# Kernel tuning notes

Measured on AMD Instinct MI355X. Metric: run time of the kernel, lower is better.

The kernel has to match this reference:

```python
import jax, jax.numpy as jnp
from jax import lax
import numpy as np

BATCH, SEQ_LEN, ENC_IN, C_OUT = 16, 512, 32, 32
N_ORDER = 256           # window_size
MULTISCALE = (1, 2, 4)
MODES = min(32, SEQ_LEN // 2)  # = 32


def make_hippo(N, dt):
    """HiPPO-LegT transition, bilinear (Tustin) discretization, Legendre eval matrix."""
    Q = np.arange(N, dtype=np.float64)
    R = (2 * Q + 1)[:, None]
    j, i = np.meshgrid(Q, Q)
    A = np.where(i < j, -1.0, (-1.0) ** (i - j + 1)) * R
    B = (-1.0) ** Q[:, None] * R                      # [N,1]
    I = np.eye(N)
    M = I - (dt / 2.0) * A
    Ad = np.linalg.solve(M, I + (dt / 2.0) * A)
    Bd = np.linalg.solve(M, dt * B).squeeze(-1)       # [N]
    vals = np.arange(0.0, 1.0, dt)
    x = 1.0 - 2.0 * vals
    P = np.zeros((N, len(vals)))
    P[0] = 1.0
    if N > 1:
        P[1] = x
    for n in range(1, N - 1):
        P[n + 1] = ((2 * n + 1) * x * P[n] - n * P[n - 1]) / (n + 1)
    E = P.T                                           # [len(vals), N]
    return Ad.astype(np.float32), Bd.astype(np.float32), E.astype(np.float32)


def setup_inputs():
    key = jax.random.key(0)
    ks = jax.random.split(key, 12)
    inp = {}
    inp['x_enc'] = jax.random.normal(ks[0], (BATCH, SEQ_LEN, ENC_IN), jnp.float32)
    inp['x_mark_enc'] = jax.random.normal(ks[1], (BATCH, SEQ_LEN, 4), jnp.float32)
    inp['x_dec'] = jax.random.normal(ks[2], (BATCH, SEQ_LEN, ENC_IN), jnp.float32)
    inp['x_mark_dec'] = jax.random.normal(ks[3], (BATCH, SEQ_LEN, 4), jnp.float32)
    inp['affine_weight'] = jnp.ones((1, 1, ENC_IN), jnp.float32)
    inp['affine_bias'] = jnp.zeros((1, 1, ENC_IN), jnp.float32)
    scale = 1.0 / (N_ORDER * N_ORDER)
    for s in range(3):
        inp[f'wr{s}'] = scale * jax.random.uniform(ks[4 + 2 * s], (N_ORDER, N_ORDER, MODES), jnp.float32)
        inp[f'wi{s}'] = scale * jax.random.uniform(ks[5 + 2 * s], (N_ORDER, N_ORDER, MODES), jnp.float32)
    inp['mlp_w'] = 0.1 * jax.random.normal(ks[10], (1, 3), jnp.float32)
    inp['mlp_b'] = jnp.zeros((1,), jnp.float32)
    inp['proj_w'] = 0.02 * jax.random.normal(ks[11], (ENC_IN, C_OUT), jnp.float32)
    inp['proj_b'] = jnp.zeros((C_OUT,), jnp.float32)
    for s, m in enumerate(MULTISCALE):
        A, Bv, E = make_hippo(N_ORDER, 1.0 / SEQ_LEN / m)
        inp[f'A{s}'] = jnp.asarray(A)
        inp[f'Bv{s}'] = jnp.asarray(Bv)
        inp[f'E{s}'] = jnp.asarray(E)
    return inp


def _hippo_scan(x, A, Bv):
    # x: [B, L, C] -> cs: [L, B, C, N]; c_t = A c_{t-1} + B f_t (applied on last dim)
    B_, L, C = x.shape
    c0 = jnp.zeros((B_, C, A.shape[0]), x.dtype)
    At = A.T
    def step(c, f):                      # f: [B, C]
        c = c @ At + f[..., None] * Bv
        return c, c
    _, cs = lax.scan(step, c0, jnp.transpose(x, (1, 0, 2)))
    return cs


def _spectral_conv(xc, wr, wi):
    # xc: [B, C, N, L]; keep first MODES rfft bins, complex channel mix over N, irfft
    L = xc.shape[-1]
    xf = jnp.fft.rfft(xc)                                # [B,C,N,L//2+1] complex64
    W = (wr + 1j * wi).astype(jnp.complex64)             # [N,N,MODES]
    out = jnp.einsum('bjix,iox->bjox', xf[..., :MODES], W)
    out_ft = jnp.pad(out, ((0, 0), (0, 0), (0, 0), (0, L // 2 + 1 - MODES)))
    return jnp.fft.irfft(out_ft, n=L)                    # [B,C,N,L]


def _forward(x_enc, affine_weight, affine_bias, specs, mlp_w, mlp_b, proj_w, proj_b, hippos):
    means = lax.stop_gradient(jnp.mean(x_enc, axis=1, keepdims=True))
    xc = x_enc - means
    stdev = lax.stop_gradient(jnp.sqrt(jnp.var(xc, axis=1, keepdims=True) + 1e-5))
    x = xc / stdev
    x = x * affine_weight + affine_bias                  # [B, L, C]
    pred_len = SEQ_LEN
    decs = []
    for (wr, wi), (A, Bv, E) in zip(specs, hippos):
        # multiscale slice x[:, -m*pred_len:] clips to full seq_len since pred_len==seq_len
        cs = _hippo_scan(x, A, Bv)                       # [L,B,C,N]
        x_in_c = jnp.transpose(cs, (1, 2, 3, 0))         # [B,C,N,L]
        out1 = _spectral_conv(x_in_c, wr, wi)            # [B,C,N,L]
        x_dec_c = out1[..., pred_len - 1]                # [B,C,N]
        dec = x_dec_c @ E[-pred_len:, :].T               # [B,C,pred_len]
        decs.append(dec)
    stacked = jnp.stack(decs, axis=-1)                   # [B,C,P,3]
    y = stacked @ mlp_w[0] + mlp_b[0]                    # Linear(3,1) + squeeze -> [B,C,P]
    y = jnp.transpose(y, (0, 2, 1))                      # [B,P,C]
    y = (y - affine_bias) / (affine_weight + 1e-10)
    y = y * stdev + means
    return y @ proj_w + proj_b                           # OutputBlock: per-step channel projection


def reference(x_enc, x_mark_enc, x_dec, x_mark_dec, affine_weight, affine_bias,
              wr0, wi0, wr1, wi1, wr2, wi2, mlp_w, mlp_b, proj_w, proj_b,
              A0, Bv0, E0, A1, Bv1, E1, A2, Bv2, E2):
    specs = [(wr0, wi0), (wr1, wi1), (wr2, wi2)]
    hippos = [(A0, Bv0, E0), (A1, Bv1, E1), (A2, Bv2, E2)]
    return _forward(x_enc, affine_weight, affine_bias, specs, mlp_w, mlp_b, proj_w, proj_b, hippos)
```

## Files before the change

### kernel.cpp

```cpp
#include <hip/hip_runtime.h>
#include <math.h>

#define SEQ 512
#define NORD 256
#define MODES 32
#define KBIG (NORD*MODES*2)
#define PI_F 3.14159265358979323846f

typedef _Float16 half8 __attribute__((ext_vector_type(8)));
typedef float floatx4 __attribute__((ext_vector_type(4)));


struct GJob {
  const float* A; const float* B; float* C; const float* scale_ptr;
  int M, N, lda, k0, k1, atomic;
};
struct GJobs { GJob j[6]; };

__global__ __launch_bounds__(256) void gemm32_k(GJobs P) {
  GJob jb = P.j[blockIdx.z];
  int col0 = blockIdx.x * 32;
  int row0 = blockIdx.y * 32;
  if (row0 >= jb.M || col0 >= jb.N) return;
  __shared__ float As[64][34];
  __shared__ float Bs[64][36];
  int tid = threadIdx.x;
  int tx = tid & 15, ty = tid >> 4;
  const float* A = jb.A; const float* B = jb.B;
  int M = jb.M, N = jb.N, lda = jb.lda;
  int kcA = (tid & 15) * 4, rA = tid >> 4;
  int ccB = (tid & 7) * 4, kkB = tid >> 3;
  int gr0 = row0 + rA, gr1 = row0 + rA + 16;
  const float4 z4 = make_float4(0.f, 0.f, 0.f, 0.f);
  float4 a0, a1, b0, b1;
  {
    int kb = jb.k0;
    a0 = (gr0 < M) ? *(const float4*)&A[(size_t)gr0 * lda + kb + kcA] : z4;
    a1 = (gr1 < M) ? *(const float4*)&A[(size_t)gr1 * lda + kb + kcA] : z4;
    b0 = *(const float4*)&B[(size_t)(kb + kkB) * N + col0 + ccB];
    b1 = *(const float4*)&B[(size_t)(kb + kkB + 32) * N + col0 + ccB];
  }
  float acc00 = 0.f, acc01 = 0.f, acc10 = 0.f, acc11 = 0.f;
  for (int kb = jb.k0; kb < jb.k1; kb += 64) {
    As[kcA+0][rA] = a0.x; As[kcA+1][rA] = a0.y; As[kcA+2][rA] = a0.z; As[kcA+3][rA] = a0.w;
    As[kcA+0][rA+16] = a1.x; As[kcA+1][rA+16] = a1.y; As[kcA+2][rA+16] = a1.z; As[kcA+3][rA+16] = a1.w;
    *(float4*)&Bs[kkB][ccB] = b0;
    *(float4*)&Bs[kkB+32][ccB] = b1;
    __syncthreads();
    if (kb + 64 < jb.k1) {
      int kn = kb + 64;
      a0 = (gr0 < M) ? *(const float4*)&A[(size_t)gr0 * lda + kn + kcA] : z4;
      a1 = (gr1 < M) ? *(const float4*)&A[(size_t)gr1 * lda + kn + kcA] : z4;
      b0 = *(const float4*)&B[(size_t)(kn + kkB) * N + col0 + ccB];
      b1 = *(const float4*)&B[(size_t)(kn + kkB + 32) * N + col0 + ccB];
    }
    #pragma unroll
    for (int k = 0; k < 64; k++) {
      float2 av = *(float2*)&As[k][ty * 2];
      float2 bv = *(float2*)&Bs[k][tx * 2];
      acc00 += av.x * bv.x; acc01 += av.x * bv.y;
      acc10 += av.y * bv.x; acc11 += av.y * bv.y;
    }
    __syncthreads();
  }
  float sc = jb.scale_ptr ? *jb.scale_ptr : 1.f;
  int gr = row0 + ty * 2, gc = col0 + tx * 2;
  float v00 = acc00 * sc, v01 = acc01 * sc, v10 = acc10 * sc, v11 = acc11 * sc;
  if (jb.atomic) {
    if (gr < M)     { atomicAdd(&jb.C[(size_t)gr * N + gc], v00);     atomicAdd(&jb.C[(size_t)gr * N + gc + 1], v01); }
    if (gr + 1 < M) { atomicAdd(&jb.C[(size_t)(gr+1) * N + gc], v10); atomicAdd(&jb.C[(size_t)(gr+1) * N + gc + 1], v11); }
  } else {
    if (gr < M)     { jb.C[(size_t)gr * N + gc] = v00;     jb.C[(size_t)gr * N + gc + 1] = v01; }
    if (gr + 1 < M) { jb.C[(size_t)(gr+1) * N + gc] = v10; jb.C[(size_t)(gr+1) * N + gc + 1] = v11; }
  }
}


__global__ __launch_bounds__(256) void prep2_k(const float* __restrict__ x_enc,
                                               const float* __restrict__ aw,
                                               const float* __restrict__ ab,
                                               float* __restrict__ F,
                                               float* __restrict__ stats,
                                               const float* A0, const float* A1, const float* A2,
                                               const float* B0, const float* B1, const float* B2,
                                               const float* E0, const float* E1, const float* E2,
                                               float* R, float* Kry, float* Et, float* Z,
                                               const float* wr0, const float* wi0,
                                               const float* wr1, const float* wi1,
                                               const float* wr2, const float* wi2,
                                               _Float16* __restrict__ Wt) {
  __shared__ float tile[32][33];
  __shared__ float ws1[4], ws2[4];
  __shared__ float mean_s, istd_s;
  int bid = blockIdx.x;
  int tid = threadIdx.x;
  if (bid < 512) {
    int row = bid;
    int b = row >> 5, c = row & 31;
    const float* xp = x_enc + (size_t)b * SEQ * 32 + c;
    float v0 = xp[(size_t)tid * 32];
    float v1 = xp[(size_t)(tid + 256) * 32];
    float s = v0 + v1, s2 = v0 * v0 + v1 * v1;
    for (int off = 32; off; off >>= 1) {
      s  += __shfl_down(s,  off, 64);
      s2 += __shfl_down(s2, off, 64);
    }
    int wid = tid >> 6, lane = tid & 63;
    if (lane == 0) { ws1[wid] = s; ws2[wid] = s2; }
    __syncthreads();
    if (tid == 0) {
      float t1 = ws1[0] + ws1[1] + ws1[2] + ws1[3];
      float t2 = ws2[0] + ws2[1] + ws2[2] + ws2[3];
      float mean = t1 / 512.f;
      float var = t2 / 512.f - mean * mean;
      float sd = sqrtf(var + 1e-5f);
      mean_s = mean; istd_s = 1.f / sd;
      stats[row] = mean; stats[512 + row] = sd;
    }
    __syncthreads();
    float w = aw[c], bb = ab[c];
    float m = mean_s, is = istd_s;
    F[(size_t)row * SEQ + tid]       = (v0 - m) * is * w + bb;
    F[(size_t)row * SEQ + tid + 256] = (v1 - m) * is * w + bb;
  } else if (bid < 704) {
    int b2 = bid - 512;
    int scl = b2 >> 6, t = b2 & 63;
    int ti = t >> 3, tm = t & 7;
    const float* A = scl == 0 ? A0 : (scl == 1 ? A1 : A2);
    float* Rd = R + (size_t)scl * 2 * 65536;
    int tx = tid & 31, ty0 = tid >> 5;
    int i0 = ti * 32, m0 = tm * 32;
    #pragma unroll
    for (int r = 0; r < 4; r++) {
      int ty = ty0 + r * 8;
      tile[ty][tx] = A[(size_t)(i0 + ty) * 256 + m0 + tx];
    }
    __syncthreads();
    #pragma unroll
    for (int r = 0; r < 4; r++) {
      int ty = ty0 + r * 8;
      Rd[(size_t)(m0 + ty) * 256 + i0 + tx] = tile[tx][ty];
    }
  } else if (bid < 1088) {
    int b2 = bid - 704;
    int scl = b2 >> 7, t = b2 & 127;
    int tp = t >> 3, to = t & 7;
    const float* E; int rows;
    if (scl == 0) { E = E0; rows = 512; }
    else if (scl == 1) { E = E1; rows = 1024; }
    else { E = E2; rows = 2048; }
    int base = rows - 512;
    int p0 = tp * 32, o0 = to * 32;
    int tx = tid & 31, ty0 = tid >> 5;
    #pragma unroll
    for (int r = 0; r < 4; r++) {
      int ty = ty0 + r * 8;
      tile[ty][tx] = E[(size_t)(base + p0 + ty) * 256 + o0 + tx];
    }
    __syncthreads();
    #pragma unroll
    for (int r = 0; r < 4; r++) {
      int ty = ty0 + r * 8;
      Et[(size_t)scl * 131072 + (size_t)(o0 + ty) * 512 + p0 + tx] = tile[tx][ty];
    }
  } else if (bid < 1091) {
    int scl = bid - 1088;
    const float* B = scl == 0 ? B0 : (scl == 1 ? B1 : B2);
    Kry[(size_t)scl * 512 * 256 + tid] = B[tid];
  } else if (bid < 1731) {
    int idx = (bid - 1091) * 256 + tid;
    ((float4*)Z)[idx] = make_float4(0.f, 0.f, 0.f, 0.f);
  } else {
    int bg = bid - 1731;
    int slab = bg >> 8;
    int s = slab;
    int r = bg & 255;
    int og = r >> 3, iq = r & 7;
    const float* wr = s == 0 ? wr0 : (s == 1 ? wr1 : wr2);
    const float* wi = s == 0 ? wi0 : (s == 1 ? wi1 : wi2);
    unsigned int* Wd = (unsigned int*)(Wt + (size_t)slab * 4194304);
    int ol = tid >> 5, k = tid & 31;
    int o = og * 8 + ol;
    float sn, cn; __sincosf((2.f * PI_F / 512.f) * (float)k, &sn, &cn);
    float g = ((k == 0) ? (1.f / 512.f) : (2.f / 512.f)) * 4096.f;
    float gc = g * cn, gs = g * sn;
    size_t obase = (size_t)(o >> 4) * 512;
    int osub = (((k >> 2) & 3) * 16 + (o & 15)) * 4 + (k & 3);
    for (int ii = 0; ii < 32; ii++) {
      int i = iq * 32 + ii;
      float a = wr[(size_t)i * 8192 + o * 32 + k];
      float b = wi[(size_t)i * 8192 + o * 32 + k];
      float v0 = gc * a + gs * b;
      float v1 = gs * a - gc * b;
      _Float16 h0 = (_Float16)v0, h1 = (_Float16)v1;
      unsigned short u0, u1;
      __builtin_memcpy(&u0, &h0, 2); __builtin_memcpy(&u1, &h1, 2);
      Wd[(obase + (size_t)(i * 2 + (k >> 4))) * 256 + osub] = (unsigned int)u0 | ((unsigned int)u1 << 16);
    }
  }
}


__global__ __launch_bounds__(256) void qbuildB_k(const float* __restrict__ Kry,
                                                 const float2* __restrict__ Pp,
                                                 _Float16* __restrict__ Qf, int s0) {
  int bg = blockIdx.x;
  int slab = bg >> 8;
  int s = s0 + slab;
  int r = bg & 255;
  int ig = r & 31, c = r >> 5;
  const float* Kry_s = Kry + (size_t)s * 131072;
  const float2* P = Pp + (size_t)s * 65536;
  uint4* Qd4 = (uint4*)(Qf + (size_t)slab * 8388608);
  int tid = threadIdx.x;
  int k = tid & 31, il = tid >> 5;
  int i = ig * 8 + il;
  __shared__ __align__(16) unsigned int buf[16 * 260];
  __shared__ float2 tbl[512];
  {
    const float step = 2.f * PI_F / 512.f;
    for (int t = tid; t < 512; t += 256) {
      float sn, cn; __sincosf(step * (float)t, &sn, &cn);
      tbl[t] = make_float2(cn, -sn);
    }
  }
  __syncthreads();
  float ar = 0.f, ai = 0.f;
  for (int cp = 0; cp < c; cp++) {
    float2 p = P[(size_t)(cp * 32 + k) * 256 + i];
    ar += p.x; ai += p.y;
  }
  int m0 = c * 64;
  int st_low = tid & 15;
  int part_base = tid >> 4;
  for (int mb = 0; mb < 64; mb += 16) {
    #pragma unroll
    for (int mm = 0; mm < 16; mm++) {
      int m = m0 + mb + mm;
      float kap = Kry_s[(size_t)m * 256 + i];
      float2 cs = tbl[(k * m) & 511];
      ar += kap * cs.x; ai += kap * cs.y;
      int st = 511 - m;
      float2 cs2 = tbl[(k * st) & 511];
      float cn2 = cs2.x, sn2 = -cs2.y;
      float qr = ar * cn2 + ai * sn2;
      float qi = ai * cn2 - ar * sn2;
      qr = fminf(fmaxf(qr, -60000.f), 60000.f);
      qi = fminf(fmaxf(qi, -60000.f), 60000.f);
      _Float16 h0 = (_Float16)qr, h1 = (_Float16)qi;
      unsigned short u0, u1;
      __builtin_memcpy(&u0, &h0, 2); __builtin_memcpy(&u1, &h1, 2);
      buf[(st & 15) * 260 + il * 32 + k] = (unsigned int)u0 | ((unsigned int)u1 << 16);
    }
    __syncthreads();
    int st_base = 496 - m0 - mb;
    int st = st_base + st_low;
    size_t rowbase = (size_t)(st >> 4) * 512;
    #pragma unroll
    for (int p = 0; p < 4; p++) {
      int part = part_base + p * 16;
      int ilw = part >> 3, k4 = part & 7;
      int iw = ig * 8 + ilw;
      size_t g = (rowbase + (size_t)(iw * 2 + (k4 >> 2))) * 64
               + (size_t)((k4 & 3) * 16 + st_low);
      Qd4[g] = *(const uint4*)&buf[st_low * 260 + ilw * 32 + k4 * 4];
    }
    __syncthreads();
  }
}


__global__ __launch_bounds__(256) void qw_k(const float* __restrict__ Kry,
                                            float2* __restrict__ Pp,
                                            const float* wr0, const float* wi0,
                                            const float* wr1, const float* wi1,
                                            const float* wr2, const float* wi2,
                                            _Float16* __restrict__ Wt, int s0, int nA) {
  __shared__ float2 tbl[512];
  int bid = blockIdx.x;
  int tid = threadIdx.x;
  if (bid < nA) {
    {
      const float step = 2.f * PI_F / 512.f;
      for (int t = tid; t < 512; t += 256) {
        float sn, cn; __sincosf(step * (float)t, &sn, &cn);
        tbl[t] = make_float2(cn, -sn);
      }
    }
    __syncthreads();
    int bg = bid;
    int s = s0 + (bg >> 8);
    int r = bg & 255;
    int k = r & 31, c = r >> 5;
    const float* Kry_s = Kry + (size_t)s * 131072;
    float2* P = Pp + (size_t)s * 65536;
    int i = tid;
    float ar = 0.f, ai = 0.f;
    int m0 = c * 64;
    for (int mm = 0; mm < 64; mm++) {
      int m = m0 + mm;
      float kap = Kry_s[(size_t)m * 256 + i];
      float2 cs = tbl[(k * m) & 511];
      ar += kap * cs.x; ai += kap * cs.y;
    }
    P[(size_t)(c * 32 + k) * 256 + i] = make_float2(ar, ai);
  } else {
    int bg = bid - nA;
    int slab = bg >> 8;
    int s = s0 + slab;
    int r = bg & 255;
    int og = r >> 3, iq = r & 7;
    const float* wr = s == 0 ? wr0 : (s == 1 ? wr1 : wr2);
    const float* wi = s == 0 ? wi0 : (s == 1 ? wi1 : wi2);
    unsigned int* Wd = (unsigned int*)(Wt + (size_t)slab * 4194304);
    int ol = tid >> 5, k = tid & 31;
    int o = og * 8 + ol;
    float sn, cn; __sincosf((2.f * PI_F / 512.f) * (float)k, &sn, &cn);
    float g = ((k == 0) ? (1.f / 512.f) : (2.f / 512.f)) * 4096.f;
    float gc = g * cn, gs = g * sn;
    size_t obase = (size_t)(o >> 4) * 512;
    int osub = (((k >> 2) & 3) * 16 + (o & 15)) * 4 + (k & 3);
    for (int ii = 0; ii < 32; ii++) {
      int i = iq * 32 + ii;
      float a = wr[(size_t)i * 8192 + o * 32 + k];
      float b = wi[(size_t)i * 8192 + o * 32 + k];
      float v0 = gc * a + gs * b;
      float v1 = gs * a - gc * b;
      _Float16 h0 = (_Float16)v0, h1 = (_Float16)v1;
      unsigned short u0, u1;
      __builtin_memcpy(&u0, &h0, 2); __builtin_memcpy(&u1, &h1, 2);
      Wd[(obase + (size_t)(i * 2 + (k >> 4))) * 256 + osub] = (unsigned int)u0 | ((unsigned int)u1 << 16);
    }
  }
}


__global__ __launch_bounds__(256) void umfma_k(const _Float16* __restrict__ Qf,
                                               const _Float16* __restrict__ Wt,
                                               float* __restrict__ U, int s0) {
  __shared__ __align__(16) _Float16 lds[2][12288];
  int kslab = blockIdx.x;
  int y = blockIdx.y;
  int slab = blockIdx.z;
  int s = s0 + slab;
  int mtb = y >> 1, ntb = y & 1;
  const _Float16* Q = Qf + (size_t)slab * 8388608;
  const _Float16* W = Wt + (size_t)slab * 4194304;
  float* Us = U + (size_t)s * 131072;
  int tid = threadIdx.x;
  int w = tid >> 6, lane = tid & 63;
  int wm = w >> 1, wn = w & 1;
  int quad = lane >> 4, lm = lane & 15;
  int mt0g = mtb * 4;
  int nt0g = ntb * 8;
  int ktg0 = kslab * 32;
  size_t laneoff = (size_t)lane * 8;

  floatx4 acc[2][4];
  #pragma unroll
  for (int a = 0; a < 2; a++)
    #pragma unroll
    for (int b = 0; b < 4; b++) acc[a][b] = (floatx4)(0.f);

  auto stage = [&](int ks, int bufi) {
    int ktg = ktg0 + ks * 2;
    #pragma unroll
    for (int q = 0; q < 6; q++) {
      int f = w * 6 + q;
      const _Float16* src;
      if (f < 8) {
        src = Q + (((size_t)(mt0g + (f >> 1)) * 512) + (size_t)(ktg + (f & 1))) * 512;
      } else {
        int g = f - 8;
        src = W + (((size_t)(nt0g + (g >> 1)) * 512) + (size_t)(ktg + (g & 1))) * 512;
      }
      __builtin_amdgcn_global_load_lds(
          (const __attribute__((address_space(1))) unsigned int*)(src + laneoff),
          (__attribute__((address_space(3))) unsigned int*)&lds[bufi][f * 512],
          16, 0, 0);
    }
  };

  stage(0, 0);
  __syncthreads();
  int buf = 0;
  for (int ks = 0; ks < 16; ks++) {
    if (ks < 15) stage(ks + 1, buf ^ 1);
    half8 a[2][2], b[4][2];
    #pragma unroll
    for (int mi2 = 0; mi2 < 2; mi2++)
      #pragma unroll
      for (int kk = 0; kk < 2; kk++)
        a[mi2][kk] = *(const half8*)&lds[buf][(size_t)(((wm * 2 + mi2) * 2 + kk) * 512) + laneoff];
    #pragma unroll
    for (int ni2 = 0; ni2 < 4; ni2++)
      #pragma unroll
      for (int kk = 0; kk < 2; kk++)
        b[ni2][kk] = *(const half8*)&lds[buf][(size_t)(4096 + ((wn * 4 + ni2) * 2 + kk) * 512) + laneoff];
    #pragma unroll
    for (int kk = 0; kk < 2; kk++)
      #pragma unroll
      for (int mi2 = 0; mi2 < 2; mi2++)
        #pragma unroll
        for (int ni2 = 0; ni2 < 4; ni2++)
          acc[mi2][ni2] = __builtin_amdgcn_mfma_f32_16x16x32_f16(a[mi2][kk], b[ni2][kk], acc[mi2][ni2], 0, 0, 0);
    __syncthreads();
    buf ^= 1;
  }

  const float sc = 1.f / 4096.f;
  #pragma unroll
  for (int mi2 = 0; mi2 < 2; mi2++) {
    int R0 = (mt0g + wm * 2 + mi2) * 16 + quad * 4;
    #pragma unroll
    for (int ni2 = 0; ni2 < 4; ni2++) {
      int gc = (nt0g + wn * 4 + ni2) * 16 + lm;
      #pragma unroll
      for (int rr2 = 0; rr2 < 4; rr2++)
        atomicAdd(&Us[(size_t)(R0 + rr2) * 256 + gc], acc[mi2][ni2][rr2] * sc);
    }
  }
}


__global__ __launch_bounds__(256) void y0final_k(const float* __restrict__ F,
                                                 const float* __restrict__ Ttot,
                                                 const float* __restrict__ stats,
                                                 const float* __restrict__ aw,
                                                 const float* __restrict__ ab,
                                                 const float* __restrict__ mlp_b,
                                                 const float* __restrict__ pw,
                                                 const float* __restrict__ pb,
                                                 float* __restrict__ out) {
  __shared__ float As[64][34];
  __shared__ float Bs[64][36];
  __shared__ float ys[32][33];
  __shared__ float pws[1024];
  int b = blockIdx.y;
  int col0 = blockIdx.x * 32;
  int row0 = b * 32;
  int tid = threadIdx.x;
  for (int t = tid; t < 1024; t += 256) pws[t] = pw[t];
  int tx = tid & 15, ty = tid >> 4;
  int kcA = (tid & 15) * 4, rA = tid >> 4;
  int ccB = (tid & 7) * 4, kkB = tid >> 3;
  int gr0 = row0 + rA, gr1 = row0 + rA + 16;
  float4 a0, a1, b0, b1;
  a0 = *(const float4*)&F[(size_t)gr0 * 512 + kcA];
  a1 = *(const float4*)&F[(size_t)gr1 * 512 + kcA];
  b0 = *(const float4*)&Ttot[(size_t)kkB * 512 + col0 + ccB];
  b1 = *(const float4*)&Ttot[(size_t)(kkB + 32) * 512 + col0 + ccB];
  float acc00 = 0.f, acc01 = 0.f, acc10 = 0.f, acc11 = 0.f;
  for (int kb = 0; kb < 512; kb += 64) {
    As[kcA+0][rA] = a0.x; As[kcA+1][rA] = a0.y; As[kcA+2][rA] = a0.z; As[kcA+3][rA] = a0.w;
    As[kcA+0][rA+16] = a1.x; As[kcA+1][rA+16] = a1.y; As[kcA+2][rA+16] = a1.z; As[kcA+3][rA+16] = a1.w;
    *(float4*)&Bs[kkB][ccB] = b0;
    *(float4*)&Bs[kkB+32][ccB] = b1;
    __syncthreads();
    if (kb + 64 < 512) {
      int kn = kb + 64;
      a0 = *(const float4*)&F[(size_t)gr0 * 512 + kn + kcA];
      a1 = *(const float4*)&F[(size_t)gr1 * 512 + kn + kcA];
      b0 = *(const float4*)&Ttot[(size_t)(kn + kkB) * 512 + col0 + ccB];
      b1 = *(const float4*)&Ttot[(size_t)(kn + kkB + 32) * 512 + col0 + ccB];
    }
    #pragma unroll
    for (int k = 0; k < 64; k++) {
      float2 av = *(float2*)&As[k][ty * 2];
      float2 bv = *(float2*)&Bs[k][tx * 2];
      acc00 += av.x * bv.x; acc01 += av.x * bv.y;
      acc10 += av.y * bv.x; acc11 += av.y * bv.y;
    }
    __syncthreads();
  }
  {
    int c0 = ty * 2, p0 = tx * 2;
    float mb0 = mlp_b[0];
    int r0 = row0 + c0;
    float mean0 = stats[r0],     sd0 = stats[512 + r0];
    float mean1 = stats[r0 + 1], sd1 = stats[512 + r0 + 1];
    float ia0 = 1.f / (aw[c0] + 1e-10f),     ab0 = ab[c0];
    float ia1 = 1.f / (aw[c0 + 1] + 1e-10f), ab1 = ab[c0 + 1];
    ys[c0][p0]     = ((acc00 + mb0) - ab0) * ia0 * sd0 + mean0;
    ys[c0][p0+1]   = ((acc01 + mb0) - ab0) * ia0 * sd0 + mean0;
    ys[c0+1][p0]   = ((acc10 + mb0) - ab1) * ia1 * sd1 + mean1;
    ys[c0+1][p0+1] = ((acc11 + mb0) - ab1) * ia1 * sd1 + mean1;
  }
  __syncthreads();
  {
    int co = tid & 31, pb2 = tid >> 5;
    #pragma unroll
    for (int q = 0; q < 4; q++) {
      int p = pb2 + q * 8;
      float accv = pb[co];
      #pragma unroll
      for (int cc = 0; cc < 32; cc++) accv += ys[cc][p] * pws[cc * 32 + co];
      out[((size_t)b * 512 + col0 + p) * 32 + co] = accv;
    }
  }
}


extern "C" void kernel_launch(void* const* d_in, const int* in_sizes, int n_in,
                              void* d_out, int out_size, void* d_ws, size_t ws_size,
                              hipStream_t stream) {
  const float* x_enc = (const float*)d_in[0];
  const float* aw = (const float*)d_in[4];
  const float* ab = (const float*)d_in[5];
  const float* wr[3] = {(const float*)d_in[6], (const float*)d_in[8], (const float*)d_in[10]};
  const float* wi[3] = {(const float*)d_in[7], (const float*)d_in[9], (const float*)d_in[11]};
  const float* mlp_w = (const float*)d_in[12];
  const float* mlp_b = (const float*)d_in[13];
  const float* proj_w = (const float*)d_in[14];
  const float* proj_b = (const float*)d_in[15];
  const float* Am[3]  = {(const float*)d_in[16], (const float*)d_in[19], (const float*)d_in[22]};
  const float* Bv[3]  = {(const float*)d_in[17], (const float*)d_in[20], (const float*)d_in[23]};
  const float* Em[3]  = {(const float*)d_in[18], (const float*)d_in[21], (const float*)d_in[24]};

  float* w = (float*)d_ws;
  float* F     = w; w += 512 * 512;
  float* stats = w; w += 1024;
  float* Kry   = w; w += 3 * 512 * 256;
  float* R     = w; w += 3 * 2 * 65536;
  float* U     = w; w += 3 * 512 * 256;
  float* Ttot  = w; w += 512 * 512;
  float* Et    = w; w += 3 * 256 * 512;
  float* y0    = w; w += 512 * 512;
  float* Pp    = w; w += 3 * 65536 * 2;
  _Float16* Qf = (_Float16*)w;

  size_t base_bytes = (size_t)((char*)Qf - (char*)d_ws);
  size_t slab_bytes = (size_t)(8388608 + 4194304) * 2;
  int nS = (ws_size >= base_bytes + 3 * slab_bytes) ? 3 : 1;
  _Float16* Wb = Qf + (size_t)nS * 8388608;
  (void)y0;

  int nW = (nS == 3) ? 768 : 0;
  prep2_k<<<1731 + nW, 256, 0, stream>>>(x_enc, aw, ab, F, stats,
                                         Am[0], Am[1], Am[2], Bv[0], Bv[1], Bv[2],
                                         Em[0], Em[1], Em[2], R, Kry, Et, U,
                                         wr[0], wi[0], wr[1], wi[1], wr[2], wi[2], Wb);

  for (int j = 0; j < 9; j++) {
    GJobs P{};
    int M = 1 << j;
    int cur = j & 1;
    int nz = 0;
    for (int s = 0; s < 3; s++) {
      float* Ks = Kry + (size_t)s * 131072;
      float* Rj = R + (size_t)s * 131072 + (size_t)cur * 65536;
      float* Rn = R + (size_t)s * 131072 + (size_t)(1 - cur) * 65536;
      P.j[nz++] = {Ks, Rj, Ks + (size_t)M * 256, nullptr, M, 256, 256, 0, 256, 0};
      if (j < 8) P.j[nz++] = {Rj, Rj, Rn, nullptr, 256, 256, 256, 0, 256, 0};
    }
    gemm32_k<<<dim3(8, 8, nz), 256, 0, stream>>>(P);
  }

  if (nS == 3) {
    qw_k<<<768, 256, 0, stream>>>(Kry, (float2*)Pp, wr[0], wi[0], wr[1], wi[1],
                                  wr[2], wi[2], Wb, 0, 768);
    qbuildB_k<<<768, 256, 0, stream>>>(Kry, (const float2*)Pp, Qf, 0);
    umfma_k<<<dim3(16, 16, 3), 256, 0, stream>>>(Qf, Wb, U, 0);
  } else {
    for (int s = 0; s < 3; s++) {
      qw_k<<<512, 256, 0, stream>>>(Kry, (float2*)Pp, wr[0], wi[0], wr[1], wi[1],
                                    wr[2], wi[2], Wb, s, 256);
      qbuildB_k<<<256, 256, 0, stream>>>(Kry, (const float2*)Pp, Qf, s);
      umfma_k<<<dim3(16, 16, 1), 256, 0, stream>>>(Qf, Wb, U, s);
    }
  }

  {
    GJobs P{};
    for (int s = 0; s < 3; s++)
      P.j[s] = {U + (size_t)s * 131072, Et + (size_t)s * 131072, Ttot,
                mlp_w + s, 512, 512, 256, 0, 256, 1};
    gemm32_k<<<dim3(16, 16, 3), 256, 0, stream>>>(P);
  }

  y0final_k<<<dim3(16, 16), 256, 0, stream>>>(F, Ttot, stats, aw, ab, mlp_b,
                                              proj_w, proj_b, (float*)d_out);
}
```

Before: 350.0 us.

## Replace split-K atomic accumulation with partial buffers and last-block reduction

The split-K MFMA kernel no longer atomically adds its 16 K-slab partial results into U. Each block now writes its partial tile to a scratch buffer, then takes a ticket on a per-tile counter, and the last-arriving block sums all 16 partials and writes U with plain stores. This removes float atomic traffic and contention on U. The cost is extra scratch memory traffic, threadfences, and a serial reduction in one block per tile. Tickets are zeroed in prep2_k. In the nS==1 path the tile index uses the local slab, so counters and the scratch buffer are reused across launches, which relies on the reset.

New measurement: 473.3 us. 1.35x slower.

```diff
diff --git a/kernel.cpp b/kernel.cpp
--- a/kernel.cpp
+++ b/kernel.cpp
@@ -85,6 +85,7 @@
                                                const float* B0, const float* B1, const float* B2,
                                                const float* E0, const float* E1, const float* E2,
                                                float* R, float* Kry, float* Et, float* Z,
+                                               unsigned* __restrict__ tick,
                                                const float* wr0, const float* wi0,
                                                const float* wr1, const float* wi1,
                                                const float* wr2, const float* wi2,
@@ -167,6 +168,7 @@
     int scl = bid - 1088;
     const float* B = scl == 0 ? B0 : (scl == 1 ? B1 : B2);
     Kry[(size_t)scl * 512 * 256 + tid] = B[tid];
+    if (bid == 1088 && tid < 64) tick[tid] = 0u;
   } else if (bid < 1731) {
     int idx = (bid - 1091) * 256 + tid;
     ((float4*)Z)[idx] = make_float4(0.f, 0.f, 0.f, 0.f);
@@ -337,8 +339,11 @@
 
 __global__ __launch_bounds__(256) void umfma_k(const _Float16* __restrict__ Qf,
                                                const _Float16* __restrict__ Wt,
-                                               float* __restrict__ U, int s0) {
+                                               float* __restrict__ U,
+                                               float* __restrict__ Upart,
+                                               unsigned* __restrict__ tick, int s0) {
   __shared__ __align__(16) _Float16 lds[2][12288];
+  __shared__ int ticket_s;
   int kslab = blockIdx.x;
   int y = blockIdx.y;
   int slab = blockIdx.z;
@@ -408,17 +413,41 @@
     buf ^= 1;
   }
 
-  const float sc = 1.f / 4096.f;
+  int tileIdx = slab * 16 + y;
+  float* myp = Upart + ((size_t)tileIdx * 16 + kslab) * 8192;
   #pragma unroll
   for (int mi2 = 0; mi2 < 2; mi2++) {
-    int R0 = (mt0g + wm * 2 + mi2) * 16 + quad * 4;
+    int lr0 = (wm * 2 + mi2) * 16 + quad * 4;
     #pragma unroll
     for (int ni2 = 0; ni2 < 4; ni2++) {
-      int gc = (nt0g + wn * 4 + ni2) * 16 + lm;
+      int lc = (wn * 4 + ni2) * 16 + lm;
       #pragma unroll
       for (int rr2 = 0; rr2 < 4; rr2++)
-        atomicAdd(&Us[(size_t)(R0 + rr2) * 256 + gc], acc[mi2][ni2][rr2] * sc);
-    }
+        myp[(size_t)(lr0 + rr2) * 128 + lc] = acc[mi2][ni2][rr2];
+    }
+  }
+  __threadfence();
+  __syncthreads();
+  if (tid == 0) ticket_s = (int)atomicAdd(&tick[tileIdx], 1u);
+  __syncthreads();
+  if (ticket_s == 15) {
+    __threadfence();
+    const float4* pbase = (const float4*)(Upart + (size_t)tileIdx * 16 * 8192);
+    const float sc = 1.f / 4096.f;
+    #pragma unroll
+    for (int e = 0; e < 8; e++) {
+      int i = e * 256 + tid;
+      float4 acc4 = pbase[i];
+      #pragma unroll
+      for (int p = 1; p < 16; p++) {
+        float4 t = pbase[(size_t)p * 2048 + i];
+        acc4.x += t.x; acc4.y += t.y; acc4.z += t.z; acc4.w += t.w;
+      }
+      acc4.x *= sc; acc4.y *= sc; acc4.z *= sc; acc4.w *= sc;
+      int lr = i >> 5, lc4 = i & 31;
+      *(float4*)&Us[(size_t)(mtb * 64 + lr) * 256 + ntb * 128 + lc4 * 4] = acc4;
+    }
+    if (tid == 0) tick[tileIdx] = 0u;
   }
 }
 
@@ -527,6 +556,8 @@
   float* Et    = w; w += 3 * 256 * 512;
   float* y0    = w; w += 512 * 512;
   float* Pp    = w; w += 3 * 65536 * 2;
+  float* Upart = w; w += 768 * 8192;
+  unsigned* tick = (unsigned*)w; w += 64;
   _Float16* Qf = (_Float16*)w;
 
   size_t base_bytes = (size_t)((char*)Qf - (char*)d_ws);
@@ -538,7 +569,7 @@
   int nW = (nS == 3) ? 768 : 0;
   prep2_k<<<1731 + nW, 256, 0, stream>>>(x_enc, aw, ab, F, stats,
                                          Am[0], Am[1], Am[2], Bv[0], Bv[1], Bv[2],
-                                         Em[0], Em[1], Em[2], R, Kry, Et, U,
+                                         Em[0], Em[1], Em[2], R, Kry, Et, U, tick,
                                          wr[0], wi[0], wr[1], wi[1], wr[2], wi[2], Wb);
 
   for (int j = 0; j < 9; j++) {
@@ -560,13 +591,13 @@
     qw_k<<<768, 256, 0, stream>>>(Kry, (float2*)Pp, wr[0], wi[0], wr[1], wi[1],
                                   wr[2], wi[2], Wb, 0, 768);
     qbuildB_k<<<768, 256, 0, stream>>>(Kry, (const float2*)Pp, Qf, 0);
-    umfma_k<<<dim3(16, 16, 3), 256, 0, stream>>>(Qf, Wb, U, 0);
+    umfma_k<<<dim3(16, 16, 3), 256, 0, stream>>>(Qf, Wb, U, Upart, tick, 0);
   } else {
     for (int s = 0; s < 3; s++) {
       qw_k<<<512, 256, 0, stream>>>(Kry, (float2*)Pp, wr[0], wi[0], wr[1], wi[1],
                                     wr[2], wi[2], Wb, s, 256);
       qbuildB_k<<<256, 256, 0, stream>>>(Kry, (const float2*)Pp, Qf, s);
-      umfma_k<<<dim3(16, 16, 1), 256, 0, stream>>>(Qf, Wb, U, s);
+      umfma_k<<<dim3(16, 16, 1), 256, 0, stream>>>(Qf, Wb, U, Upart, tick, s);
     }
   }
 
```
